# Kernel tuning notes

Hardware: AMD Instinct MI355X
Metric: run time of the kernel (lower is better)

The kernel has to match this reference:

```python
import jax, jax.numpy as jnp
import numpy as np

D_K = 64  # per-head dim, hardcoded in the original module


def setup_inputs() -> dict:
    key = jax.random.key(0)
    kq, kk, kv, km = jax.random.split(key, 4)
    B, H, S, D = 4, 16, 2048, 64
    Q = jax.random.normal(kq, (B, H, S, D), dtype=jnp.float32)
    K = jax.random.normal(kk, (B, H, S, D), dtype=jnp.float32)
    V = jax.random.normal(kv, (B, H, S, D), dtype=jnp.float32)
    attn_mask = jax.random.randint(km, (B, H, S, S), 0, 2).astype(jnp.bool_)
    return {"Q": Q, "K": K, "V": V, "attn_mask": attn_mask}


def reference(Q, K, V, attn_mask):
    # scores = Q @ K^T / sqrt(d_k)  -> [B, H, S, S]
    scale = 1.0 / np.sqrt(D_K).astype(np.float32)
    scores = jnp.einsum("bhqd,bhkd->bhqk", Q, K) * scale
    scores = jnp.where(attn_mask, jnp.float32(-1e9), scores)
    attn = jax.nn.softmax(scores, axis=-1)
    context = jnp.einsum("bhqk,bhkd->bhqd", attn, V)
    return (context, attn)
```

## Files before the change

### kernel.cpp

```cpp
#include <hip/hip_runtime.h>
#include <stdint.h>

#define S_LEN 2048
#define D_HEAD 64
#define NBH 64
#define QBLK 32
#define KBLK 64
#define NITER (S_LEN / KBLK)

typedef __attribute__((ext_vector_type(8))) short short8;
typedef __attribute__((ext_vector_type(4))) float f32x4;

#define KB_OFF 0
#define VT_OFF 16384
#define P_OFF  24576
#define MB_OFF 28672
#define LP_OFF 36864
#define SMEM_BYTES 37120

__device__ __forceinline__ int swz1(int row, int b) {
  return row * 128 + (b ^ ((row & 7) << 4));
}
__device__ __forceinline__ int swz2(int row, int b) {
  return row * 128 + (b ^ (((row >> 1) & 7) << 4));
}

__device__ __forceinline__ short f2b(float x) {
  unsigned u = __float_as_uint(x);
  unsigned r = 0x7FFFu + ((u >> 16) & 1u);
  return (short)((u + r) >> 16);
}
__device__ __forceinline__ float b2f(short s) {
  return __uint_as_float(((unsigned)(unsigned short)s) << 16);
}

__device__ __forceinline__ void gload_lds16(const void* g, void* l) {
  __builtin_amdgcn_global_load_lds(
      (const __attribute__((address_space(1))) unsigned int*)g,
      (__attribute__((address_space(3))) unsigned int*)l, 16, 0, 0);
}

__global__ void detect_mask_kernel(const unsigned* m, int* flag) {
  unsigned v = m[blockIdx.x * 256 + threadIdx.x];
  if (v != 0u && v != 1u && v != 0x3F800000u) atomicOr(flag, 1);
}

__global__ void __launch_bounds__(256) convK_kernel(
    const float* __restrict__ in, short* __restrict__ out) {
  size_t i = ((size_t)blockIdx.x * 256 + threadIdx.x) * 8;
  float4 a = ((const float4*)(in + i))[0];
  float4 b = ((const float4*)(in + i))[1];
  short8 v;
  v[0] = f2b(a.x); v[1] = f2b(a.y); v[2] = f2b(a.z); v[3] = f2b(a.w);
  v[4] = f2b(b.x); v[5] = f2b(b.y); v[6] = f2b(b.z); v[7] = f2b(b.w);
  *(short8*)(out + i) = v;
}

__global__ void __launch_bounds__(256) convVT_kernel(
    const float* __restrict__ V, short* __restrict__ out) {
  __shared__ __align__(16) short t[64 * 72];
  int tid = threadIdx.x;
  int kb = blockIdx.x * 64, bh = blockIdx.y;
  const float* src = V + ((size_t)bh * S_LEN + kb) * D_HEAD;
#pragma unroll
  for (int j = 0; j < 4; ++j) {
    int key = j * 16 + (tid >> 4), d0 = (tid & 15) * 4;
    float4 f = *(const float4*)(src + (size_t)key * D_HEAD + d0);
    t[(d0 + 0) * 72 + key] = f2b(f.x);
    t[(d0 + 1) * 72 + key] = f2b(f.y);
    t[(d0 + 2) * 72 + key] = f2b(f.z);
    t[(d0 + 3) * 72 + key] = f2b(f.w);
  }
  __syncthreads();
  int row = tid >> 2, seg = tid & 3;
  short8 v0 = *(const short8*)(t + row * 72 + seg * 16);
  short8 v1 = *(const short8*)(t + row * 72 + seg * 16 + 8);
  short* dst = out + (size_t)bh * D_HEAD * S_LEN + (size_t)row * S_LEN + kb + seg * 16;
  *(short8*)dst = v0;
  *(short8*)(dst + 8) = v1;
}

template <bool BYTEMASK, bool PRE>
__device__ __forceinline__ void attn_body(
    char* smem, const float* Qg, const float* Kg, const float* Vg,
    const void* maskg, const short* Kbf, const short* Vtb,
    float* ctxg, float* attng) {

  const int tid = threadIdx.x;
  const int w = tid >> 6, l = tid & 63;
  const int lg = l >> 4, li = l & 15;
  const int rh = w >> 1, ch = w & 1;
  const int qb = blockIdx.x, bh = blockIdx.y;
  const int qbase = qb * QBLK;

  const float* Qp = Qg + ((size_t)bh * S_LEN + qbase) * D_HEAD;
  const float* Kp = Kg + (size_t)bh * S_LEN * D_HEAD;
  const float* Vp = Vg + (size_t)bh * S_LEN * D_HEAD;
  const short* Kbp = Kbf + (size_t)bh * S_LEN * D_HEAD;
  const short* Vtp = Vtb + (size_t)bh * D_HEAD * S_LEN;
  float* attnp = attng + ((size_t)bh * S_LEN + qbase) * S_LEN;
  float* ctxp  = ctxg  + ((size_t)bh * S_LEN + qbase) * D_HEAD;
  const size_t mrow0 = ((size_t)bh * S_LEN + qbase) * S_LEN;

  auto stageK = [&](int it, int buf) {
    char* kb = smem + KB_OFF + buf * 8192;
    if constexpr (PRE) {
      const int r0 = w * 16 + (l >> 3), ci = l & 7;
#pragma unroll
      for (int j = 0; j < 2; ++j) {
        int r = r0 + j * 8;
        const short* src = Kbp + ((size_t)(it * KBLK + r)) * D_HEAD + ((ci ^ (r & 7)) * 8);
        int off = __builtin_amdgcn_readfirstlane((w * 16 + j * 8) * 128);
        gload_lds16(src, kb + off);
      }
    } else {
      int key = tid >> 2, seg = tid & 3;
      const float* src = Kp + ((size_t)(it * KBLK + key)) * D_HEAD + seg * 16;
      float4 f0 = ((const float4*)src)[0];
      float4 f1 = ((const float4*)src)[1];
      float4 f2 = ((const float4*)src)[2];
      float4 f3 = ((const float4*)src)[3];
      short8 v0, v1;
      v0[0] = f2b(f0.x); v0[1] = f2b(f0.y); v0[2] = f2b(f0.z); v0[3] = f2b(f0.w);
      v0[4] = f2b(f1.x); v0[5] = f2b(f1.y); v0[6] = f2b(f1.z); v0[7] = f2b(f1.w);
      v1[0] = f2b(f2.x); v1[1] = f2b(f2.y); v1[2] = f2b(f2.z); v1[3] = f2b(f2.w);
      v1[4] = f2b(f3.x); v1[5] = f2b(f3.y); v1[6] = f2b(f3.z); v1[7] = f2b(f3.w);
      *(short8*)(kb + swz1(key, seg * 32)) = v0;
      *(short8*)(kb + swz1(key, seg * 32 + 16)) = v1;
    }
  };

  auto stageVt = [&](int it) {
    char* vb = smem + VT_OFF;
    if constexpr (PRE) {
      const int d0 = w * 16 + (l >> 3), ci = l & 7;
#pragma unroll
      for (int j = 0; j < 2; ++j) {
        int d = d0 + j * 8;
        const short* src = Vtp + (size_t)d * S_LEN + it * KBLK + ((ci ^ (d & 7)) * 8);
        int off = __builtin_amdgcn_readfirstlane((w * 16 + j * 8) * 128);
        gload_lds16(src, vb + off);
      }
    } else {
      int key = l, db = w;
      const float* src = Vp + ((size_t)(it * KBLK + key)) * D_HEAD + db * 16;
#pragma unroll
      for (int j = 0; j < 4; ++j) {
        float4 f = ((const float4*)src)[j];
        int dd = db * 16 + j * 4;
        *(short*)(vb + swz1(dd + 0, key * 2)) = f2b(f.x);
        *(short*)(vb + swz1(dd + 1, key * 2)) = f2b(f.y);
        *(short*)(vb + swz1(dd + 2, key * 2)) = f2b(f.z);
        *(short*)(vb + swz1(dd + 3, key * 2)) = f2b(f.w);
      }
    }
  };

  auto loadMask = [&](int it, unsigned* m) {
#pragma unroll
    for (int reg = 0; reg < 4; ++reg) {
      int row = rh * 16 + lg * 4 + reg;
#pragma unroll
      for (int ct = 0; ct < 2; ++ct) {
        size_t idx = mrow0 + (size_t)row * S_LEN + it * KBLK + ch * 32 + ct * 16 + li;
        if constexpr (BYTEMASK)
          m[ct * 4 + reg] = (unsigned)((const unsigned char*)maskg)[idx];
        else
          m[ct * 4 + reg] = ((const unsigned*)maskg)[idx];
      }
    }
  };

  auto qkt = [&](f32x4* accs, const short8* qf, int buf) {
    char* kb = smem + KB_OFF + buf * 8192;
#pragma unroll
    for (int ct = 0; ct < 2; ++ct) {
      int key = ch * 32 + ct * 16 + li;
      short8 b0 = *(const short8*)(kb + swz1(key, lg * 16));
      short8 b1 = *(const short8*)(kb + swz1(key, 64 + lg * 16));
      accs[ct] = __builtin_amdgcn_mfma_f32_16x16x32_bf16(qf[0], b0, accs[ct], 0, 0, 0);
      accs[ct] = __builtin_amdgcn_mfma_f32_16x16x32_bf16(qf[1], b1, accs[ct], 0, 0, 0);
    }
  };

  stageK(0, 0);
  unsigned mc[8];
  loadMask(0, mc);
  {
    int row = tid >> 3, seg = tid & 7;
    const float* src = Qp + row * D_HEAD + seg * 8;
    float4 a = ((const float4*)src)[0];
    float4 b = ((const float4*)src)[1];
    short8 v;
    v[0] = f2b(a.x); v[1] = f2b(a.y); v[2] = f2b(a.z); v[3] = f2b(a.w);
    v[4] = f2b(b.x); v[5] = f2b(b.y); v[6] = f2b(b.z); v[7] = f2b(b.w);
    *(short8*)(smem + P_OFF + swz1(row, seg * 16)) = v;
  }
  __syncthreads();
  short8 qfrag[2];
  {
    int row = rh * 16 + li;
    qfrag[0] = *(const short8*)(smem + P_OFF + swz1(row, lg * 16));
    qfrag[1] = *(const short8*)(smem + P_OFF + swz1(row, 64 + lg * 16));
  }
  __syncthreads();

  float l_acc[4] = {0.f, 0.f, 0.f, 0.f};
  for (int it = 0; it < NITER; ++it) {
    const int cb = it & 1, nb = cb ^ 1;
    if (it + 1 < NITER) stageK(it + 1, nb);
    unsigned mn[8];
    if (it + 1 < NITER) loadMask(it + 1, mn);
    f32x4 accs[2] = {{0.f,0.f,0.f,0.f},{0.f,0.f,0.f,0.f}};
    qkt(accs, qfrag, cb);
    unsigned mbyte = 0;
#pragma unroll
    for (int reg = 0; reg < 4; ++reg) {
      float contrib = 0.f;
#pragma unroll
      for (int ct = 0; ct < 2; ++ct) {
        bool pred = mc[ct * 4 + reg] != 0u;
        mbyte |= (unsigned)pred << (ct * 4 + reg);
        float p = pred ? 0.f : __expf(accs[ct][reg] * 0.125f);
        contrib += p;
      }
      contrib += __shfl_xor(contrib, 1);
      contrib += __shfl_xor(contrib, 2);
      contrib += __shfl_xor(contrib, 4);
      contrib += __shfl_xor(contrib, 8);
      l_acc[reg] += contrib;
    }
    *(unsigned char*)(smem + MB_OFF + it * 256 + tid) = (unsigned char)mbyte;
    __syncthreads();
    if (it + 1 < NITER) {
#pragma unroll
      for (int i = 0; i < 8; ++i) mc[i] = mn[i];
    }
  }

  if (li == 0) {
#pragma unroll
    for (int reg = 0; reg < 4; ++reg)
      *(float*)(smem + LP_OFF + ch * 128 + (rh * 16 + lg * 4 + reg) * 4) = l_acc[reg];
  }
  stageK(0, 0);
  stageVt(0);
  __syncthreads();
  float linv[4];
#pragma unroll
  for (int reg = 0; reg < 4; ++reg) {
    int row = rh * 16 + lg * 4 + reg;
    float tot = *(const float*)(smem + LP_OFF + row * 4) +
                *(const float*)(smem + LP_OFF + 128 + row * 4);
    linv[reg] = 1.0f / tot;
  }

  f32x4 acco[2] = {{0.f,0.f,0.f,0.f},{0.f,0.f,0.f,0.f}};
  for (int it = 0; it < NITER; ++it) {
    const int cb = it & 1, nb = cb ^ 1;
    if (it > 0) stageVt(it);
    if (it + 1 < NITER) stageK(it + 1, nb);
    f32x4 accs[2] = {{0.f,0.f,0.f,0.f},{0.f,0.f,0.f,0.f}};
    qkt(accs, qfrag, cb);
    unsigned mbyte = *(const unsigned char*)(smem + MB_OFF + it * 256 + tid);
#pragma unroll
    for (int reg = 0; reg < 4; ++reg) {
      int row = rh * 16 + lg * 4 + reg;
#pragma unroll
      for (int ct = 0; ct < 2; ++ct) {
        int col = ch * 32 + ct * 16 + li;
        bool pred = (mbyte >> (ct * 4 + reg)) & 1u;
        float p = pred ? 0.f : __expf(accs[ct][reg] * 0.125f) * linv[reg];
        *(short*)(smem + P_OFF + swz2(row, col * 2)) = f2b(p);
      }
    }
    __syncthreads();
    {
      int row = tid >> 3, seg = tid & 7;
      short8 pv = *(const short8*)(smem + P_OFF + swz2(row, seg * 16));
      float* dst = attnp + (size_t)row * S_LEN + it * KBLK + seg * 8;
      float4 f0, f1;
      f0.x = b2f(pv[0]); f0.y = b2f(pv[1]); f0.z = b2f(pv[2]); f0.w = b2f(pv[3]);
      f1.x = b2f(pv[4]); f1.y = b2f(pv[5]); f1.z = b2f(pv[6]); f1.w = b2f(pv[7]);
      ((float4*)dst)[0] = f0;
      ((float4*)dst)[1] = f1;
    }
#pragma unroll
    for (int ks = 0; ks < 2; ++ks) {
      int prow = rh * 16 + li;
      short8 af = *(const short8*)(smem + P_OFF + swz2(prow, ks * 64 + lg * 16));
#pragma unroll
      for (int ct2 = 0; ct2 < 2; ++ct2) {
        int d = ch * 32 + ct2 * 16 + li;
        short8 bf = *(const short8*)(smem + VT_OFF + swz1(d, ks * 64 + lg * 16));
        acco[ct2] = __builtin_amdgcn_mfma_f32_16x16x32_bf16(af, bf, acco[ct2], 0, 0, 0);
      }
    }
    __syncthreads();
  }

#pragma unroll
  for (int ct2 = 0; ct2 < 2; ++ct2) {
#pragma unroll
    for (int reg = 0; reg < 4; ++reg) {
      int row = rh * 16 + lg * 4 + reg;
      int d = ch * 32 + ct2 * 16 + li;
      ctxp[(size_t)row * D_HEAD + d] = acco[ct2][reg];
    }
  }
}

template <bool PRE>
__global__ void __launch_bounds__(256, 4)
attn_kernel(const float* Q, const float* K, const float* V, const void* M,
            const short* Kbf, const short* Vtb,
            float* ctx, float* attn, const int* flag) {
  extern __shared__ char smem[];
  if (*flag)
    attn_body<true, PRE>(smem, Q, K, V, M, Kbf, Vtb, ctx, attn);
  else
    attn_body<false, PRE>(smem, Q, K, V, M, Kbf, Vtb, ctx, attn);
}

extern "C" void kernel_launch(void* const* d_in, const int* in_sizes, int n_in,
                              void* d_out, int out_size, void* d_ws, size_t ws_size,
                              hipStream_t stream) {
  const float* Q = (const float*)d_in[0];
  const float* K = (const float*)d_in[1];
  const float* V = (const float*)d_in[2];
  const void*  M = d_in[3];
  float* ctx  = (float*)d_out;
  float* attn = ctx + (size_t)NBH * S_LEN * D_HEAD;
  int* flag = (int*)d_ws;
  short* Kbf = (short*)((char*)d_ws + 256);
  short* Vtb = Kbf + (size_t)NBH * S_LEN * D_HEAD;
  const size_t PRE_BYTES = 256 + (size_t)2 * NBH * S_LEN * D_HEAD * sizeof(short);

  hipMemsetAsync(flag, 0, sizeof(int), stream);
  detect_mask_kernel<<<dim3(16), dim3(256), 0, stream>>>((const unsigned*)M, flag);

  dim3 grid(S_LEN / QBLK, NBH);
  if (ws_size >= PRE_BYTES) {
    convK_kernel<<<dim3(4096), dim3(256), 0, stream>>>(K, Kbf);
    convVT_kernel<<<dim3(32, 64), dim3(256), 0, stream>>>(V, Vtb);
    attn_kernel<true><<<grid, dim3(256), SMEM_BYTES, stream>>>(
        Q, K, V, M, Kbf, Vtb, ctx, attn, flag);
  } else {
    attn_kernel<false><<<grid, dim3(256), SMEM_BYTES, stream>>>(
        Q, K, V, M, Kbf, Vtb, ctx, attn, flag);
  }
}
```

Measured before the change: 645.0 us.

## Add two-pass attention kernel with packed mask bits and recomputed QK^T

Adds a new attention kernel used on the precomputed-bf16 path. A first pass computes QK^T and accumulates softmax row sums, reading the mask once with coalesced vector loads and storing it as one bit per element in LDS. A second pass recomputes QK^T, writes normalized probabilities and runs the PV MFMA using double-buffered K and V^T tiles. The running max subtraction is dropped, which relies on bounded scores and can overflow or produce NaN on fully masked rows. Blocks are also remapped so that blocks for the same head are grouped together, aiming to improve L2 reuse.

```diff
diff --git a/kernel.cpp b/kernel.cpp
--- a/kernel.cpp
+++ b/kernel.cpp
@@ -11,12 +11,20 @@
 typedef __attribute__((ext_vector_type(8))) short short8;
 typedef __attribute__((ext_vector_type(4))) float f32x4;
 
-#define KB_OFF 0
+#define K_OFF  0
 #define VT_OFF 16384
 #define P_OFF  24576
 #define MB_OFF 28672
 #define LP_OFF 36864
 #define SMEM_BYTES 37120
+
+#define KB2_OFF 0
+#define VT2_OFF 16384
+#define S2_OFF  32768
+#define S1_OFF  40960
+#define P2_OFF  49152
+#define LP2_OFF 53248
+#define SMEM2_BYTES 53504
 
 __device__ __forceinline__ int swz1(int row, int b) {
   return row * 128 + (b ^ ((row & 7) << 4));
@@ -80,6 +88,236 @@
   *(short8*)(dst + 8) = v1;
 }
 
+template <bool BYTEMASK>
+__device__ __forceinline__ void attn_fast(
+    char* smem, const float* Qg, const void* maskg,
+    const short* Kbf, const short* Vtb, float* ctxg, float* attng,
+    int qb, int bh) {
+
+  const int tid = threadIdx.x;
+  const int w = tid >> 6, l = tid & 63;
+  const int lg = l >> 4, li = l & 15;
+  const int rh = w >> 1, ch = w & 1;
+  const int qbase = qb * QBLK;
+  const int row = tid >> 3, seg = tid & 7;
+  const int xr = (row & 7) << 4;
+
+  const float* Qp = Qg + ((size_t)bh * S_LEN + qbase) * D_HEAD;
+  const short* Kbp = Kbf + (size_t)bh * S_LEN * D_HEAD;
+  const short* Vtp = Vtb + (size_t)bh * D_HEAD * S_LEN;
+  float* attnp = attng + ((size_t)bh * S_LEN + qbase) * S_LEN;
+  float* ctxp  = ctxg  + ((size_t)bh * S_LEN + qbase) * D_HEAD;
+  const size_t mbase = ((size_t)bh * S_LEN + qbase + row) * S_LEN + seg * 8;
+
+  auto stageK = [&](int it, int buf) {
+    const int r0 = w * 16 + (l >> 3), ci = l & 7;
+#pragma unroll
+    for (int j = 0; j < 2; ++j) {
+      int r = r0 + j * 8;
+      const short* src = Kbp + ((size_t)(it * KBLK + r)) * D_HEAD + ((ci ^ (r & 7)) * 8);
+      int off = __builtin_amdgcn_readfirstlane(buf * 8192 + (w * 16 + j * 8) * 128);
+      gload_lds16(src, smem + KB2_OFF + off);
+    }
+  };
+  auto stageVt = [&](int it, int buf) {
+    const int d0 = w * 16 + (l >> 3), ci = l & 7;
+#pragma unroll
+    for (int j = 0; j < 2; ++j) {
+      int d = d0 + j * 8;
+      const short* src = Vtp + (size_t)d * S_LEN + it * KBLK + ((ci ^ (d & 7)) * 8);
+      int off = __builtin_amdgcn_readfirstlane(buf * 8192 + (w * 16 + j * 8) * 128);
+      gload_lds16(src, smem + VT2_OFF + off);
+    }
+  };
+
+  auto qkt = [&](f32x4* accs, const short8* qf, int buf) {
+    char* kb = smem + KB2_OFF + buf * 8192;
+#pragma unroll
+    for (int ct = 0; ct < 2; ++ct) {
+      int key = ch * 32 + ct * 16 + li;
+      short8 b0 = *(const short8*)(kb + swz1(key, lg * 16));
+      short8 b1 = *(const short8*)(kb + swz1(key, 64 + lg * 16));
+      accs[ct] = __builtin_amdgcn_mfma_f32_16x16x32_bf16(qf[0], b0, accs[ct], 0, 0, 0);
+      accs[ct] = __builtin_amdgcn_mfma_f32_16x16x32_bf16(qf[1], b1, accs[ct], 0, 0, 0);
+    }
+  };
+
+  auto writeS = [&](int sb, const f32x4* accs) {
+    char* sbuf = smem + S2_OFF + sb * 8192;
+#pragma unroll
+    for (int ct = 0; ct < 2; ++ct)
+#pragma unroll
+      for (int reg = 0; reg < 4; ++reg) {
+        int rw = rh * 16 + lg * 4 + reg;
+        int col = ch * 32 + ct * 16 + li;
+        *(float*)(sbuf + rw * 256 + ((col * 4) ^ ((rw & 7) << 4))) = accs[ct][reg];
+      }
+  };
+
+  struct MaskRegs { int4 a, b; uint2 c; };
+  auto loadMask = [&](int it, MaskRegs& m) {
+    if constexpr (BYTEMASK) {
+      m.c = *(const uint2*)((const unsigned char*)maskg + mbase + it * KBLK);
+    } else {
+      const int* p = (const int*)maskg + mbase + it * KBLK;
+      m.a = *(const int4*)p;
+      m.b = *(const int4*)(p + 4);
+    }
+  };
+  auto predByte = [&](const MaskRegs& m) -> unsigned {
+    unsigned pb = 0;
+    if constexpr (BYTEMASK) {
+      unsigned lo = m.c.x, hi = m.c.y;
+#pragma unroll
+      for (int j = 0; j < 4; ++j) {
+        pb |= (((lo >> (8 * j)) & 255u) != 0u ? 1u : 0u) << j;
+        pb |= (((hi >> (8 * j)) & 255u) != 0u ? 1u : 0u) << (j + 4);
+      }
+    } else {
+      pb |= (m.a.x != 0) ? 1u : 0u;
+      pb |= (m.a.y != 0) ? 2u : 0u;
+      pb |= (m.a.z != 0) ? 4u : 0u;
+      pb |= (m.a.w != 0) ? 8u : 0u;
+      pb |= (m.b.x != 0) ? 16u : 0u;
+      pb |= (m.b.y != 0) ? 32u : 0u;
+      pb |= (m.b.z != 0) ? 64u : 0u;
+      pb |= (m.b.w != 0) ? 128u : 0u;
+    }
+    return pb;
+  };
+
+  stageK(0, 0);
+  MaskRegs mc; loadMask(0, mc);
+  {
+    const float* src = Qp + row * D_HEAD + seg * 8;
+    float4 a = ((const float4*)src)[0];
+    float4 b = ((const float4*)src)[1];
+    short8 v;
+    v[0] = f2b(a.x); v[1] = f2b(a.y); v[2] = f2b(a.z); v[3] = f2b(a.w);
+    v[4] = f2b(b.x); v[5] = f2b(b.y); v[6] = f2b(b.z); v[7] = f2b(b.w);
+    *(short8*)(smem + P2_OFF + row * 128 + ((seg * 16) ^ xr)) = v;
+  }
+  __syncthreads();
+  short8 qfrag[2];
+  {
+    int qr = rh * 16 + li;
+    int xq = (qr & 7) << 4;
+    qfrag[0] = *(const short8*)(smem + P2_OFF + qr * 128 + ((lg * 16) ^ xq));
+    qfrag[1] = *(const short8*)(smem + P2_OFF + qr * 128 + ((64 + lg * 16) ^ xq));
+  }
+  __syncthreads();
+
+  float l_acc = 0.f;
+  for (int it = 0; it < NITER; ++it) {
+    const int cb = it & 1, nb = cb ^ 1;
+    MaskRegs mn;
+    if (it + 1 < NITER) { stageK(it + 1, nb); loadMask(it + 1, mn); }
+    f32x4 accs[2] = {{0.f,0.f,0.f,0.f},{0.f,0.f,0.f,0.f}};
+    qkt(accs, qfrag, cb);
+    writeS(cb, accs);
+    __syncthreads();
+    char* sbuf = smem + S2_OFF + cb * 8192;
+    float4 s0 = *(const float4*)(sbuf + row * 256 + ((seg * 32) ^ xr));
+    float4 s1 = *(const float4*)(sbuf + row * 256 + ((seg * 32 + 16) ^ xr));
+    unsigned pb = predByte(mc);
+    float sum = 0.f;
+    sum += (pb & 1u)   ? 0.f : __expf(s0.x * 0.125f);
+    sum += (pb & 2u)   ? 0.f : __expf(s0.y * 0.125f);
+    sum += (pb & 4u)   ? 0.f : __expf(s0.z * 0.125f);
+    sum += (pb & 8u)   ? 0.f : __expf(s0.w * 0.125f);
+    sum += (pb & 16u)  ? 0.f : __expf(s1.x * 0.125f);
+    sum += (pb & 32u)  ? 0.f : __expf(s1.y * 0.125f);
+    sum += (pb & 64u)  ? 0.f : __expf(s1.z * 0.125f);
+    sum += (pb & 128u) ? 0.f : __expf(s1.w * 0.125f);
+    l_acc += sum;
+    *(unsigned char*)(smem + VT2_OFF + it * 256 + tid) = (unsigned char)pb;
+    if (it + 1 < NITER) mc = mn;
+  }
+
+  l_acc += __shfl_xor(l_acc, 1);
+  l_acc += __shfl_xor(l_acc, 2);
+  l_acc += __shfl_xor(l_acc, 4);
+  if (seg == 0) *(float*)(smem + LP2_OFF + row * 4) = l_acc;
+  __syncthreads();
+  float4 pc0 = *(const float4*)(smem + VT2_OFF + tid * 32);
+  float4 pc1 = *(const float4*)(smem + VT2_OFF + tid * 32 + 16);
+  float linv = 1.0f / *(const float*)(smem + LP2_OFF + row * 4);
+  *(float4*)(smem + S1_OFF + tid * 32) = pc0;
+  *(float4*)(smem + S1_OFF + tid * 32 + 16) = pc1;
+  __syncthreads();
+  stageK(0, 0);
+  stageVt(0, 0);
+  __syncthreads();
+
+  f32x4 acco[2] = {{0.f,0.f,0.f,0.f},{0.f,0.f,0.f,0.f}};
+  for (int it = 0; it < NITER; ++it) {
+    const int cb = it & 1, nb = cb ^ 1;
+    if (it + 1 < NITER) stageK(it + 1, nb);
+    unsigned pb = *(const unsigned char*)(smem + S1_OFF + it * 256 + tid);
+    f32x4 accs[2] = {{0.f,0.f,0.f,0.f},{0.f,0.f,0.f,0.f}};
+    qkt(accs, qfrag, cb);
+    writeS(0, accs);
+    __syncthreads();
+    if (it + 1 < NITER) stageVt(it + 1, nb);
+    {
+      char* sbuf = smem + S2_OFF;
+      float4 s0 = *(const float4*)(sbuf + row * 256 + ((seg * 32) ^ xr));
+      float4 s1 = *(const float4*)(sbuf + row * 256 + ((seg * 32 + 16) ^ xr));
+      float4 o0, o1;
+      o0.x = (pb & 1u)   ? 0.f : __expf(s0.x * 0.125f) * linv;
+      o0.y = (pb & 2u)   ? 0.f : __expf(s0.y * 0.125f) * linv;
+      o0.z = (pb & 4u)   ? 0.f : __expf(s0.z * 0.125f) * linv;
+      o0.w = (pb & 8u)   ? 0.f : __expf(s0.w * 0.125f) * linv;
+      o1.x = (pb & 16u)  ? 0.f : __expf(s1.x * 0.125f) * linv;
+      o1.y = (pb & 32u)  ? 0.f : __expf(s1.y * 0.125f) * linv;
+      o1.z = (pb & 64u)  ? 0.f : __expf(s1.z * 0.125f) * linv;
+      o1.w = (pb & 128u) ? 0.f : __expf(s1.w * 0.125f) * linv;
+      float* dst = attnp + (size_t)row * S_LEN + it * KBLK + seg * 8;
+      ((float4*)dst)[0] = o0;
+      ((float4*)dst)[1] = o1;
+      short8 pv;
+      pv[0] = f2b(o0.x); pv[1] = f2b(o0.y); pv[2] = f2b(o0.z); pv[3] = f2b(o0.w);
+      pv[4] = f2b(o1.x); pv[5] = f2b(o1.y); pv[6] = f2b(o1.z); pv[7] = f2b(o1.w);
+      *(short8*)(smem + P2_OFF + row * 128 + ((seg * 16) ^ xr)) = pv;
+    }
+    __syncthreads();
+#pragma unroll
+    for (int ks = 0; ks < 2; ++ks) {
+      int prow = rh * 16 + li;
+      int xp = (prow & 7) << 4;
+      short8 af = *(const short8*)(smem + P2_OFF + prow * 128 + ((ks * 64 + lg * 16) ^ xp));
+#pragma unroll
+      for (int ct2 = 0; ct2 < 2; ++ct2) {
+        int d = ch * 32 + ct2 * 16 + li;
+        short8 bf = *(const short8*)(smem + VT2_OFF + cb * 8192 + swz1(d, ks * 64 + lg * 16));
+        acco[ct2] = __builtin_amdgcn_mfma_f32_16x16x32_bf16(af, bf, acco[ct2], 0, 0, 0);
+      }
+    }
+  }
+
+#pragma unroll
+  for (int ct2 = 0; ct2 < 2; ++ct2)
+#pragma unroll
+    for (int reg = 0; reg < 4; ++reg) {
+      int rw = rh * 16 + lg * 4 + reg;
+      int d = ch * 32 + ct2 * 16 + li;
+      ctxp[(size_t)rw * D_HEAD + d] = acco[ct2][reg];
+    }
+}
+
+__global__ void __launch_bounds__(256, 3)
+attn_fast_kernel(const float* Q, const void* M, const short* Kbf, const short* Vtb,
+                 float* ctx, float* attn, const int* flag) {
+  extern __shared__ char smem[];
+  int bid = blockIdx.x;
+  int s = ((bid & 7) << 9) | (bid >> 3);
+  int bh = s >> 6, qb = s & 63;
+  if (*flag)
+    attn_fast<true>(smem, Q, M, Kbf, Vtb, ctx, attn, qb, bh);
+  else
+    attn_fast<false>(smem, Q, M, Kbf, Vtb, ctx, attn, qb, bh);
+}
+
 template <bool BYTEMASK, bool PRE>
 __device__ __forceinline__ void attn_body(
     char* smem, const float* Qg, const float* Kg, const float* Vg,
@@ -103,7 +341,7 @@
   const size_t mrow0 = ((size_t)bh * S_LEN + qbase) * S_LEN;
 
   auto stageK = [&](int it, int buf) {
-    char* kb = smem + KB_OFF + buf * 8192;
+    char* kb = smem + K_OFF + buf * 8192;
     if constexpr (PRE) {
       const int r0 = w * 16 + (l >> 3), ci = l & 7;
 #pragma unroll
@@ -172,7 +410,7 @@
   };
 
   auto qkt = [&](f32x4* accs, const short8* qf, int buf) {
-    char* kb = smem + KB_OFF + buf * 8192;
+    char* kb = smem + K_OFF + buf * 8192;
 #pragma unroll
     for (int ct = 0; ct < 2; ++ct) {
       int key = ch * 32 + ct * 16 + li;
@@ -339,13 +577,13 @@
   hipMemsetAsync(flag, 0, sizeof(int), stream);
   detect_mask_kernel<<<dim3(16), dim3(256), 0, stream>>>((const unsigned*)M, flag);
 
-  dim3 grid(S_LEN / QBLK, NBH);
   if (ws_size >= PRE_BYTES) {
     convK_kernel<<<dim3(4096), dim3(256), 0, stream>>>(K, Kbf);
     convVT_kernel<<<dim3(32, 64), dim3(256), 0, stream>>>(V, Vtb);
-    attn_kernel<true><<<grid, dim3(256), SMEM_BYTES, stream>>>(
-        Q, K, V, M, Kbf, Vtb, ctx, attn, flag);
+    attn_fast_kernel<<<dim3(4096), dim3(256), SMEM2_BYTES, stream>>>(
+        Q, M, Kbf, Vtb, ctx, attn, flag);
   } else {
+    dim3 grid(S_LEN / QBLK, NBH);
     attn_kernel<false><<<grid, dim3(256), SMEM_BYTES, stream>>>(
         Q, K, V, M, Kbf, Vtb, ctx, attn, flag);
   }
```

After: 726.2 us. 12.6% more time.

## Replace block-cooperative attention with per-wave independent 16-row kernel reading K/V from global

Applied to the files above, without the earlier changes.

Adds a new attention kernel in which each wavefront independently handles 16 query rows. K and V^T fragments are read directly from global memory (bf16 pre-converted) instead of being staged through shared LDS with block barriers, and the softmax uses exp2 with the scale folded into Q. Mask bits are packed into registers in pass one and reused in pass two. Attention probabilities are now stored as full fp32 directly rather than round-tripping through bf16, and blocks are remapped for L2 locality. This removes block-wide syncs at the cost of redundant global K/V reads per wave and higher register pressure.

```diff
diff --git a/kernel.cpp b/kernel.cpp
--- a/kernel.cpp
+++ b/kernel.cpp
@@ -1,43 +1,27 @@
 #include <hip/hip_runtime.h>
+#include <hip/hip_bf16.h>
 #include <stdint.h>
 
 #define S_LEN 2048
 #define D_HEAD 64
 #define NBH 64
-#define QBLK 32
 #define KBLK 64
 #define NITER (S_LEN / KBLK)
 
+#define QSCALE 0.1803368801111244f
+
 typedef __attribute__((ext_vector_type(8))) short short8;
 typedef __attribute__((ext_vector_type(4))) float f32x4;
-
-#define KB_OFF 0
-#define VT_OFF 16384
-#define P_OFF  24576
-#define MB_OFF 28672
-#define LP_OFF 36864
-#define SMEM_BYTES 37120
-
-__device__ __forceinline__ int swz1(int row, int b) {
-  return row * 128 + (b ^ ((row & 7) << 4));
-}
-__device__ __forceinline__ int swz2(int row, int b) {
-  return row * 128 + (b ^ (((row >> 1) & 7) << 4));
-}
 
 __device__ __forceinline__ short f2b(float x) {
   unsigned u = __float_as_uint(x);
   unsigned r = 0x7FFFu + ((u >> 16) & 1u);
   return (short)((u + r) >> 16);
 }
-__device__ __forceinline__ float b2f(short s) {
-  return __uint_as_float(((unsigned)(unsigned short)s) << 16);
-}
-
-__device__ __forceinline__ void gload_lds16(const void* g, void* l) {
-  __builtin_amdgcn_global_load_lds(
-      (const __attribute__((address_space(1))) unsigned int*)g,
-      (__attribute__((address_space(3))) unsigned int*)l, 16, 0, 0);
+__device__ __forceinline__ unsigned pack2bf(float e0, float e1) {
+  union { __hip_bfloat162 h; unsigned u; } cv;
+  cv.h = __float22bfloat162_rn(float2{e0, e1});
+  return cv.u;
 }
 
 __global__ void detect_mask_kernel(const unsigned* m, int* flag) {
@@ -80,89 +64,242 @@
   *(short8*)(dst + 8) = v1;
 }
 
-template <bool BYTEMASK, bool PRE>
+template <bool BYTEMASK>
+__device__ __forceinline__ void attn_fast(
+    char* Pw, float* linvw, const float* Qg, const void* maskg,
+    const short* Kbf, const short* Vtb, float* ctxg, float* attng,
+    int g) {
+
+  const int l = threadIdx.x & 63;
+  const int li = l & 15, hi = l >> 4;
+  const int bh = g >> 7;
+  const int qbase = (g & 127) * 16;
+
+  const short* Kbp = Kbf + (size_t)bh * S_LEN * D_HEAD;
+  const short* Vtp = Vtb + (size_t)bh * D_HEAD * S_LEN;
+  const float* Qp  = Qg + ((size_t)bh * S_LEN + qbase) * D_HEAD;
+  float* arow = attng + ((size_t)bh * S_LEN + qbase + li) * S_LEN;
+  float* ctxp = ctxg + ((size_t)bh * S_LEN + qbase) * D_HEAD;
+
+  short8 qf0, qf1;
+  {
+    const float* qsrc = Qp + li * D_HEAD + hi * 8;
+    float4 a = *(const float4*)(qsrc);
+    float4 b = *(const float4*)(qsrc + 4);
+    float4 c = *(const float4*)(qsrc + 32);
+    float4 d = *(const float4*)(qsrc + 36);
+    qf0[0] = f2b(a.x * QSCALE); qf0[1] = f2b(a.y * QSCALE);
+    qf0[2] = f2b(a.z * QSCALE); qf0[3] = f2b(a.w * QSCALE);
+    qf0[4] = f2b(b.x * QSCALE); qf0[5] = f2b(b.y * QSCALE);
+    qf0[6] = f2b(b.z * QSCALE); qf0[7] = f2b(b.w * QSCALE);
+    qf1[0] = f2b(c.x * QSCALE); qf1[1] = f2b(c.y * QSCALE);
+    qf1[2] = f2b(c.z * QSCALE); qf1[3] = f2b(c.w * QSCALE);
+    qf1[4] = f2b(d.x * QSCALE); qf1[5] = f2b(d.y * QSCALE);
+    qf1[6] = f2b(d.z * QSCALE); qf1[7] = f2b(d.w * QSCALE);
+  }
+
+  const unsigned char* mrowB =
+      (const unsigned char*)maskg + (size_t)(((size_t)bh * S_LEN + qbase + li)) * S_LEN;
+  const int* mrowI = (const int*)maskg + (size_t)(((size_t)bh * S_LEN + qbase + li)) * S_LEN;
+
+  auto loadK = [&](int i, short8 kf[4][2]) {
+    const short* kb = Kbp + (size_t)i * KBLK * D_HEAD + (size_t)li * D_HEAD + hi * 8;
+#pragma unroll
+    for (int ct = 0; ct < 4; ++ct) {
+      const short* kr = kb + ct * 16 * D_HEAD;
+      kf[ct][0] = *(const short8*)(kr);
+      kf[ct][1] = *(const short8*)(kr + 32);
+    }
+  };
+
+  auto qkt = [&](const short8 kf[4][2], f32x4* sa) {
+#pragma unroll
+    for (int ct = 0; ct < 4; ++ct) {
+      f32x4 z = {0.f, 0.f, 0.f, 0.f};
+      sa[ct] = __builtin_amdgcn_mfma_f32_16x16x32_bf16(kf[ct][0], qf0, z, 0, 0, 0);
+      sa[ct] = __builtin_amdgcn_mfma_f32_16x16x32_bf16(kf[ct][1], qf1, sa[ct], 0, 0, 0);
+    }
+  };
+
+  auto loadPred = [&](int i) -> unsigned {
+    unsigned pb = 0;
+    if constexpr (BYTEMASK) {
+#pragma unroll
+      for (int ct = 0; ct < 4; ++ct) {
+        unsigned m = *(const unsigned*)(mrowB + i * KBLK + ct * 16 + hi * 4);
+        pb |= ((m * 0x01020408u) >> 24) << (ct * 4);
+      }
+    } else {
+#pragma unroll
+      for (int ct = 0; ct < 4; ++ct) {
+        int4 m = *(const int4*)(mrowI + i * KBLK + ct * 16 + hi * 4);
+        unsigned p4 = (m.x != 0 ? 1u : 0u) | (m.y != 0 ? 2u : 0u) |
+                      (m.z != 0 ? 4u : 0u) | (m.w != 0 ? 8u : 0u);
+        pb |= p4 << (ct * 4);
+      }
+    }
+    return pb;
+  };
+
+  unsigned pred[16];
+  float lsum = 0.f;
+#pragma unroll
+  for (int i = 0; i < NITER; ++i) {
+    short8 kf[4][2];
+    loadK(i, kf);
+    unsigned pb = loadPred(i);
+    f32x4 sa[4];
+    qkt(kf, sa);
+#pragma unroll
+    for (int ct = 0; ct < 4; ++ct)
+#pragma unroll
+      for (int reg = 0; reg < 4; ++reg) {
+        float e = ((pb >> (ct * 4 + reg)) & 1u) ? 0.f : exp2f(sa[ct][reg]);
+        lsum += e;
+      }
+    if (i & 1) pred[i >> 1] |= pb << 16; else pred[i >> 1] = pb;
+  }
+
+  lsum += __shfl_xor(lsum, 16);
+  lsum += __shfl_xor(lsum, 32);
+  const float linv = 1.0f / lsum;
+  if (l < 16) linvw[li] = linv;
+  float linv4[4];
+#pragma unroll
+  for (int r = 0; r < 4; ++r) linv4[r] = linvw[hi * 4 + r];
+
+  f32x4 po[4];
+#pragma unroll
+  for (int ct2 = 0; ct2 < 4; ++ct2) po[ct2] = f32x4{0.f, 0.f, 0.f, 0.f};
+
+#pragma unroll
+  for (int i = 0; i < NITER; ++i) {
+    short8 kf[4][2];
+    loadK(i, kf);
+    f32x4 sa[4];
+    qkt(kf, sa);
+    const unsigned pb = (pred[i >> 1] >> ((i & 1) * 16)) & 0xffffu;
+#pragma unroll
+    for (int ct = 0; ct < 4; ++ct) {
+      float e0 = ((pb >> (ct * 4 + 0)) & 1u) ? 0.f : exp2f(sa[ct][0]);
+      float e1 = ((pb >> (ct * 4 + 1)) & 1u) ? 0.f : exp2f(sa[ct][1]);
+      float e2 = ((pb >> (ct * 4 + 2)) & 1u) ? 0.f : exp2f(sa[ct][2]);
+      float e3 = ((pb >> (ct * 4 + 3)) & 1u) ? 0.f : exp2f(sa[ct][3]);
+      float4 st = {e0 * linv, e1 * linv, e2 * linv, e3 * linv};
+      *(float4*)(arow + i * KBLK + ct * 16 + hi * 4) = st;
+      uint2 pk;
+      pk.x = pack2bf(e0, e1);
+      pk.y = pack2bf(e2, e3);
+      *(uint2*)(Pw + li * 128 + (((ct * 2 + (hi >> 1)) ^ (li & 7)) << 4) +
+                ((hi & 1) * 8)) = pk;
+    }
+#pragma unroll
+    for (int ks = 0; ks < 2; ++ks) {
+      short8 pA = *(const short8*)(Pw + li * 128 + ((((ks * 4) + hi) ^ (li & 7)) << 4));
+#pragma unroll
+      for (int ct2 = 0; ct2 < 4; ++ct2) {
+        const short* vr = Vtp + (size_t)(ct2 * 16 + li) * S_LEN + i * KBLK + ks * 32 + hi * 8;
+        short8 vB = *(const short8*)vr;
+        po[ct2] = __builtin_amdgcn_mfma_f32_16x16x32_bf16(pA, vB, po[ct2], 0, 0, 0);
+      }
+    }
+  }
+
+#pragma unroll
+  for (int ct2 = 0; ct2 < 4; ++ct2)
+#pragma unroll
+    for (int reg = 0; reg < 4; ++reg)
+      ctxp[(size_t)(hi * 4 + reg) * D_HEAD + ct2 * 16 + li] = po[ct2][reg] * linv4[reg];
+}
+
+__global__ void __launch_bounds__(256, 3)
+attn_fast_kernel(const float* Q, const void* M, const short* Kbf, const short* Vtb,
+                 float* ctx, float* attn, const int* flag) {
+  __shared__ __align__(16) char smem[4 * 2048 + 4 * 64];
+  const int w = threadIdx.x >> 6;
+  char* Pw = smem + w * 2048;
+  float* linvw = (float*)(smem + 4 * 2048 + w * 64);
+  int bid = blockIdx.x;
+  int s = ((bid & 7) << 8) | (bid >> 3);
+  int g = s * 4 + w;
+  if (*flag)
+    attn_fast<true>(Pw, linvw, Q, M, Kbf, Vtb, ctx, attn, g);
+  else
+    attn_fast<false>(Pw, linvw, Q, M, Kbf, Vtb, ctx, attn, g);
+}
+
+#define FK_OFF  0
+#define FVT_OFF 16384
+#define FP_OFF  24576
+#define FMB_OFF 28672
+#define FLP_OFF 36864
+#define FSMEM_BYTES 37120
+
+__device__ __forceinline__ int swz1(int row, int b) {
+  return row * 128 + (b ^ ((row & 7) << 4));
+}
+__device__ __forceinline__ int swz2(int row, int b) {
+  return row * 128 + (b ^ (((row >> 1) & 7) << 4));
+}
+
+template <bool BYTEMASK>
 __device__ __forceinline__ void attn_body(
     char* smem, const float* Qg, const float* Kg, const float* Vg,
-    const void* maskg, const short* Kbf, const short* Vtb,
-    float* ctxg, float* attng) {
+    const void* maskg, float* ctxg, float* attng) {
 
   const int tid = threadIdx.x;
   const int w = tid >> 6, l = tid & 63;
   const int lg = l >> 4, li = l & 15;
   const int rh = w >> 1, ch = w & 1;
   const int qb = blockIdx.x, bh = blockIdx.y;
-  const int qbase = qb * QBLK;
+  const int qbase = qb * 32;
 
   const float* Qp = Qg + ((size_t)bh * S_LEN + qbase) * D_HEAD;
   const float* Kp = Kg + (size_t)bh * S_LEN * D_HEAD;
   const float* Vp = Vg + (size_t)bh * S_LEN * D_HEAD;
-  const short* Kbp = Kbf + (size_t)bh * S_LEN * D_HEAD;
-  const short* Vtp = Vtb + (size_t)bh * D_HEAD * S_LEN;
   float* attnp = attng + ((size_t)bh * S_LEN + qbase) * S_LEN;
   float* ctxp  = ctxg  + ((size_t)bh * S_LEN + qbase) * D_HEAD;
   const size_t mrow0 = ((size_t)bh * S_LEN + qbase) * S_LEN;
 
   auto stageK = [&](int it, int buf) {
-    char* kb = smem + KB_OFF + buf * 8192;
-    if constexpr (PRE) {
-      const int r0 = w * 16 + (l >> 3), ci = l & 7;
-#pragma unroll
-      for (int j = 0; j < 2; ++j) {
-        int r = r0 + j * 8;
-        const short* src = Kbp + ((size_t)(it * KBLK + r)) * D_HEAD + ((ci ^ (r & 7)) * 8);
-        int off = __builtin_amdgcn_readfirstlane((w * 16 + j * 8) * 128);
-        gload_lds16(src, kb + off);
-      }
-    } else {
-      int key = tid >> 2, seg = tid & 3;
-      const float* src = Kp + ((size_t)(it * KBLK + key)) * D_HEAD + seg * 16;
-      float4 f0 = ((const float4*)src)[0];
-      float4 f1 = ((const float4*)src)[1];
-      float4 f2 = ((const float4*)src)[2];
-      float4 f3 = ((const float4*)src)[3];
-      short8 v0, v1;
-      v0[0] = f2b(f0.x); v0[1] = f2b(f0.y); v0[2] = f2b(f0.z); v0[3] = f2b(f0.w);
-      v0[4] = f2b(f1.x); v0[5] = f2b(f1.y); v0[6] = f2b(f1.z); v0[7] = f2b(f1.w);
-      v1[0] = f2b(f2.x); v1[1] = f2b(f2.y); v1[2] = f2b(f2.z); v1[3] = f2b(f2.w);
-      v1[4] = f2b(f3.x); v1[5] = f2b(f3.y); v1[6] = f2b(f3.z); v1[7] = f2b(f3.w);
-      *(short8*)(kb + swz1(key, seg * 32)) = v0;
-      *(short8*)(kb + swz1(key, seg * 32 + 16)) = v1;
-    }
+    char* kb = smem + FK_OFF + buf * 8192;
+    int key = tid >> 2, seg = tid & 3;
+    const float* src = Kp + ((size_t)(it * KBLK + key)) * D_HEAD + seg * 16;
+    float4 f0 = ((const float4*)src)[0];
+    float4 f1 = ((const float4*)src)[1];
+    float4 f2 = ((const float4*)src)[2];
+    float4 f3 = ((const float4*)src)[3];
+    short8 v0, v1;
+    v0[0] = f2b(f0.x); v0[1] = f2b(f0.y); v0[2] = f2b(f0.z); v0[3] = f2b(f0.w);
+    v0[4] = f2b(f1.x); v0[5] = f2b(f1.y); v0[6] = f2b(f1.z); v0[7] = f2b(f1.w);
+    v1[0] = f2b(f2.x); v1[1] = f2b(f2.y); v1[2] = f2b(f2.z); v1[3] = f2b(f2.w);
+    v1[4] = f2b(f3.x); v1[5] = f2b(f3.y); v1[6] = f2b(f3.z); v1[7] = f2b(f3.w);
+    *(short8*)(kb + swz1(key, seg * 32)) = v0;
+    *(short8*)(kb + swz1(key, seg * 32 + 16)) = v1;
   };
 
   auto stageVt = [&](int it) {
-    char* vb = smem + VT_OFF;
-    if constexpr (PRE) {
-      const int d0 = w * 16 + (l >> 3), ci = l & 7;
-#pragma unroll
-      for (int j = 0; j < 2; ++j) {
-        int d = d0 + j * 8;
-        const short* src = Vtp + (size_t)d * S_LEN + it * KBLK + ((ci ^ (d & 7)) * 8);
-        int off = __builtin_amdgcn_readfirstlane((w * 16 + j * 8) * 128);
-        gload_lds16(src, vb + off);
-      }
-    } else {
-      int key = l, db = w;
-      const float* src = Vp + ((size_t)(it * KBLK + key)) * D_HEAD + db * 16;
-#pragma unroll
-      for (int j = 0; j < 4; ++j) {
-        float4 f = ((const float4*)src)[j];
-        int dd = db * 16 + j * 4;
-        *(short*)(vb + swz1(dd + 0, key * 2)) = f2b(f.x);
-        *(short*)(vb + swz1(dd + 1, key * 2)) = f2b(f.y);
-        *(short*)(vb + swz1(dd + 2, key * 2)) = f2b(f.z);
-        *(short*)(vb + swz1(dd + 3, key * 2)) = f2b(f.w);
-      }
+    char* vb = smem + FVT_OFF;
+    int key = l, db = w;
+    const float* src = Vp + ((size_t)(it * KBLK + key)) * D_HEAD + db * 16;
+#pragma unroll
+    for (int j = 0; j < 4; ++j) {
+      float4 f = ((const float4*)src)[j];
+      int dd = db * 16 + j * 4;
+      *(short*)(vb + swz1(dd + 0, key * 2)) = f2b(f.x);
+      *(short*)(vb + swz1(dd + 1, key * 2)) = f2b(f.y);
+      *(short*)(vb + swz1(dd + 2, key * 2)) = f2b(f.z);
+      *(short*)(vb + swz1(dd + 3, key * 2)) = f2b(f.w);
     }
   };
 
   auto loadMask = [&](int it, unsigned* m) {
 #pragma unroll
     for (int reg = 0; reg < 4; ++reg) {
-      int row = rh * 16 + lg * 4 + reg;
+      int rw = rh * 16 + lg * 4 + reg;
 #pragma unroll
       for (int ct = 0; ct < 2; ++ct) {
-        size_t idx = mrow0 + (size_t)row * S_LEN + it * KBLK + ch * 32 + ct * 16 + li;
+        size_t idx = mrow0 + (size_t)rw * S_LEN + it * KBLK + ch * 32 + ct * 16 + li;
         if constexpr (BYTEMASK)
           m[ct * 4 + reg] = (unsigned)((const unsigned char*)maskg)[idx];
         else
@@ -172,7 +309,7 @@
   };
 
   auto qkt = [&](f32x4* accs, const short8* qf, int buf) {
-    char* kb = smem + KB_OFF + buf * 8192;
+    char* kb = smem + FK_OFF + buf * 8192;
 #pragma unroll
     for (int ct = 0; ct < 2; ++ct) {
       int key = ch * 32 + ct * 16 + li;
@@ -187,21 +324,21 @@
   unsigned mc[8];
   loadMask(0, mc);
   {
-    int row = tid >> 3, seg = tid & 7;
-    const float* src = Qp + row * D_HEAD + seg * 8;
+    int rw = tid >> 3, seg = tid & 7;
+    const float* src = Qp + rw * D_HEAD + seg * 8;
     float4 a = ((const float4*)src)[0];
     float4 b = ((const float4*)src)[1];
     short8 v;
     v[0] = f2b(a.x); v[1] = f2b(a.y); v[2] = f2b(a.z); v[3] = f2b(a.w);
     v[4] = f2b(b.x); v[5] = f2b(b.y); v[6] = f2b(b.z); v[7] = f2b(b.w);
-    *(short8*)(smem + P_OFF + swz1(row, seg * 16)) = v;
+    *(short8*)(smem + FP_OFF + swz1(rw, seg * 16)) = v;
   }
   __syncthreads();
   short8 qfrag[2];
   {
-    int row = rh * 16 + li;
-    qfrag[0] = *(const short8*)(smem + P_OFF + swz1(row, lg * 16));
-    qfrag[1] = *(const short8*)(smem + P_OFF + swz1(row, 64 + lg * 16));
+    int rw = rh * 16 + li;
+    qfrag[0] = *(const short8*)(smem + FP_OFF + swz1(rw, lg * 16));
+    qfrag[1] = *(const short8*)(smem + FP_OFF + swz1(rw, 64 + lg * 16));
   }
   __syncthreads();
 
@@ -221,8 +358,8 @@
       for (int ct = 0; ct < 2; ++ct) {
         bool pred = mc[ct * 4 + reg] != 0u;
         mbyte |= (unsigned)pred << (ct * 4 + reg);
-        float p = pred ? 0.f : __expf(accs[ct][reg] * 0.125f);
-        contrib += p;
+        float pp = pred ? 0.f : __expf(accs[ct][reg] * 0.125f);
+        contrib += pp;
       }
       contrib += __shfl_xor(contrib, 1);
       contrib += __shfl_xor(contrib, 2);
@@ -230,7 +367,7 @@
       contrib += __shfl_xor(contrib, 8);
       l_acc[reg] += contrib;
     }
-    *(unsigned char*)(smem + MB_OFF + it * 256 + tid) = (unsigned char)mbyte;
+    *(unsigned char*)(smem + FMB_OFF + it * 256 + tid) = (unsigned char)mbyte;
     __syncthreads();
     if (it + 1 < NITER) {
 #pragma unroll
@@ -241,7 +378,7 @@
   if (li == 0) {
 #pragma unroll
     for (int reg = 0; reg < 4; ++reg)
-      *(float*)(smem + LP_OFF + ch * 128 + (rh * 16 + lg * 4 + reg) * 4) = l_acc[reg];
+      *(float*)(smem + FLP_OFF + ch * 128 + (rh * 16 + lg * 4 + reg) * 4) = l_acc[reg];
   }
   stageK(0, 0);
   stageVt(0);
@@ -249,10 +386,9 @@
   float linv[4];
 #pragma unroll
   for (int reg = 0; reg < 4; ++reg) {
-    int row = rh * 16 + lg * 4 + reg;
-    float tot = *(const float*)(smem + LP_OFF + row * 4) +
-                *(const float*)(smem + LP_OFF + 128 + row * 4);
-    linv[reg] = 1.0f / tot;
+    int rw = rh * 16 + lg * 4 + reg;
+    linv[reg] = 1.0f / (*(const float*)(smem + FLP_OFF + rw * 4) +
+                        *(const float*)(smem + FLP_OFF + 128 + rw * 4));
   }
 
   f32x4 acco[2] = {{0.f,0.f,0.f,0.f},{0.f,0.f,0.f,0.f}};
@@ -262,37 +398,28 @@
     if (it + 1 < NITER) stageK(it + 1, nb);
     f32x4 accs[2] = {{0.f,0.f,0.f,0.f},{0.f,0.f,0.f,0.f}};
     qkt(accs, qfrag, cb);
-    unsigned mbyte = *(const unsigned char*)(smem + MB_OFF + it * 256 + tid);
+    unsigned mbyte = *(const unsigned char*)(smem + FMB_OFF + it * 256 + tid);
 #pragma unroll
     for (int reg = 0; reg < 4; ++reg) {
-      int row = rh * 16 + lg * 4 + reg;
+      int rw = rh * 16 + lg * 4 + reg;
 #pragma unroll
       for (int ct = 0; ct < 2; ++ct) {
         int col = ch * 32 + ct * 16 + li;
         bool pred = (mbyte >> (ct * 4 + reg)) & 1u;
-        float p = pred ? 0.f : __expf(accs[ct][reg] * 0.125f) * linv[reg];
-        *(short*)(smem + P_OFF + swz2(row, col * 2)) = f2b(p);
+        float pp = pred ? 0.f : __expf(accs[ct][reg] * 0.125f) * linv[reg];
+        attnp[(size_t)rw * S_LEN + it * KBLK + col] = pp;
+        *(short*)(smem + FP_OFF + swz2(rw, col * 2)) = f2b(pp);
       }
     }
     __syncthreads();
-    {
-      int row = tid >> 3, seg = tid & 7;
-      short8 pv = *(const short8*)(smem + P_OFF + swz2(row, seg * 16));
-      float* dst = attnp + (size_t)row * S_LEN + it * KBLK + seg * 8;
-      float4 f0, f1;
-      f0.x = b2f(pv[0]); f0.y = b2f(pv[1]); f0.z = b2f(pv[2]); f0.w = b2f(pv[3]);
-      f1.x = b2f(pv[4]); f1.y = b2f(pv[5]); f1.z = b2f(pv[6]); f1.w = b2f(pv[7]);
-      ((float4*)dst)[0] = f0;
-      ((float4*)dst)[1] = f1;
-    }
 #pragma unroll
     for (int ks = 0; ks < 2; ++ks) {
       int prow = rh * 16 + li;
-      short8 af = *(const short8*)(smem + P_OFF + swz2(prow, ks * 64 + lg * 16));
+      short8 af = *(const short8*)(smem + FP_OFF + swz2(prow, ks * 64 + lg * 16));
 #pragma unroll
       for (int ct2 = 0; ct2 < 2; ++ct2) {
         int d = ch * 32 + ct2 * 16 + li;
-        short8 bf = *(const short8*)(smem + VT_OFF + swz1(d, ks * 64 + lg * 16));
+        short8 bf = *(const short8*)(smem + FVT_OFF + swz1(d, ks * 64 + lg * 16));
         acco[ct2] = __builtin_amdgcn_mfma_f32_16x16x32_bf16(af, bf, acco[ct2], 0, 0, 0);
       }
     }
@@ -303,23 +430,21 @@
   for (int ct2 = 0; ct2 < 2; ++ct2) {
 #pragma unroll
     for (int reg = 0; reg < 4; ++reg) {
-      int row = rh * 16 + lg * 4 + reg;
+      int rw = rh * 16 + lg * 4 + reg;
       int d = ch * 32 + ct2 * 16 + li;
-      ctxp[(size_t)row * D_HEAD + d] = acco[ct2][reg];
-    }
-  }
-}
-
-template <bool PRE>
+      ctxp[(size_t)rw * D_HEAD + d] = acco[ct2][reg];
+    }
+  }
+}
+
 __global__ void __launch_bounds__(256, 4)
 attn_kernel(const float* Q, const float* K, const float* V, const void* M,
-            const short* Kbf, const short* Vtb,
             float* ctx, float* attn, const int* flag) {
   extern __shared__ char smem[];
   if (*flag)
-    attn_body<true, PRE>(smem, Q, K, V, M, Kbf, Vtb, ctx, attn);
+    attn_body<true>(smem, Q, K, V, M, ctx, attn);
   else
-    attn_body<false, PRE>(smem, Q, K, V, M, Kbf, Vtb, ctx, attn);
+    attn_body<false>(smem, Q, K, V, M, ctx, attn);
 }
 
 extern "C" void kernel_launch(void* const* d_in, const int* in_sizes, int n_in,
@@ -339,14 +464,14 @@
   hipMemsetAsync(flag, 0, sizeof(int), stream);
   detect_mask_kernel<<<dim3(16), dim3(256), 0, stream>>>((const unsigned*)M, flag);
 
-  dim3 grid(S_LEN / QBLK, NBH);
   if (ws_size >= PRE_BYTES) {
     convK_kernel<<<dim3(4096), dim3(256), 0, stream>>>(K, Kbf);
     convVT_kernel<<<dim3(32, 64), dim3(256), 0, stream>>>(V, Vtb);
-    attn_kernel<true><<<grid, dim3(256), SMEM_BYTES, stream>>>(
-        Q, K, V, M, Kbf, Vtb, ctx, attn, flag);
+    attn_fast_kernel<<<dim3(2048), dim3(256), 0, stream>>>(
+        Q, M, Kbf, Vtb, ctx, attn, flag);
   } else {
-    attn_kernel<false><<<grid, dim3(256), SMEM_BYTES, stream>>>(
-        Q, K, V, M, Kbf, Vtb, ctx, attn, flag);
-  }
-}
+    dim3 grid(S_LEN / 32, NBH);
+    attn_kernel<<<grid, dim3(256), FSMEM_BYTES, stream>>>(
+        Q, K, V, M, ctx, attn, flag);
+  }
+}
```

New measurement: 1.712 ms. 165% more time.
